# Kernel optimization log

Hardware: AMD Instinct MI355X
Metric: run time of the kernel (lower is better)

## Reference

```python
import jax, jax.numpy as jnp
import numpy as np
from jax import lax

EPSILON = 0.05      # sinkhorn entropic regularization (module init arg)
N_SINKHORN = 100    # fixed iteration count (POT default numItermax=1000 w/ early stop 1e-9)


def setup_inputs() -> dict:
    key = jax.random.key(0)
    k1, k2, k3 = jax.random.split(key, 3)
    B, D = 2048, 1024
    audio_emb = jax.random.normal(k1, (B, D), dtype=jnp.float32)
    text_emb = jax.random.normal(k2, (B, D), dtype=jnp.float32)
    # learned metric L (set via set_L); PSD so diag(L) > 0 and sqrt is real
    A = jax.random.normal(k3, (D, D), dtype=jnp.float32)
    L = (A @ A.T) / jnp.float32(D)
    return {"audio_emb": audio_emb, "text_emb": text_emb, "L": L}


def reference(audio_emb, text_emb, L):
    B = audio_emb.shape[0]
    M = jnp.nan_to_num(L)
    # SVD is computed in the original (reg term), but the final loss discards it
    s = jnp.linalg.svd(M, compute_uv=False)
    _reg = jnp.sum(s)  # unused in returned loss (original: loss = wloss)

    # einsum('ijk,ikj,kk->ij') only reads diag(M):
    # M_dist[i,j] = sum_k diag(M)[k] * (audio[j,k] - text[i,k])^2
    w = jnp.diagonal(M)  # [D]
    aw = jnp.einsum('jd,d->j', audio_emb * audio_emb, w)        # [B]
    tw = jnp.einsum('id,d->i', text_emb * text_emb, w)          # [B]
    cross = jnp.einsum('id,jd->ij', text_emb * w, audio_emb)    # [B,B]
    M_dist = tw[:, None] + aw[None, :] - 2.0 * cross
    M_dist = jnp.sqrt(jnp.maximum(M_dist, 0.0))
    M_dist = M_dist / jnp.max(M_dist)

    # Sinkhorn-Knopp (ot.sinkhorn, method='sinkhorn')
    a = jnp.ones((B,), dtype=M_dist.dtype) / B
    b = jnp.ones((B,), dtype=M_dist.dtype) / B
    K = jnp.exp(-M_dist / EPSILON)  # [B,B]

    def step(uv, _):
        u, v = uv
        v = b / (K.T @ u)
        u = a / (K @ v)
        return (u, v), None

    u0 = jnp.ones((B,), dtype=M_dist.dtype) / B
    v0 = jnp.ones((B,), dtype=M_dist.dtype) / B
    (u, v), _ = lax.scan(step, (u0, v0), None, length=N_SINKHORN)
    # pi = diag(u) K diag(v); pi_hat = eye(B)/B -> only diag(pi) matters
    pi_diag = u * jnp.diagonal(K) * v  # [B]
    wloss = -jnp.sum(jnp.log(pi_diag)) / B
    return wloss
```

## Files before the change

kernel.cpp:

```cpp
#include <hip/hip_runtime.h>
#include <hip/hip_fp16.h>
#include <math.h>

#define NB 2048
#define ND 1024
#define EPS 0.05f
#define NITER 100
#define SBLK 256
#define KSCALE 16384.0f
#define LOG_KSCALE 9.704060527839234

typedef float f32x4 __attribute__((ext_vector_type(4)));
typedef float f32x2 __attribute__((ext_vector_type(2)));
typedef short s16x8 __attribute__((ext_vector_type(8)));
typedef unsigned short u16x4 __attribute__((ext_vector_type(4)));
union Uh { f32x4 f; __half2 h[4]; };

__global__ void prep_k(const float* __restrict__ L, float* __restrict__ w,
                       float* __restrict__ u, float* __restrict__ v,
                       unsigned* __restrict__ maxbits, unsigned* __restrict__ flags) {
    int gtid = blockIdx.x * 256 + threadIdx.x;
    if (gtid < ND) {
        float x = L[(size_t)gtid * (ND + 1)];
        if (x != x) x = 0.f;
        else if (fabsf(x) == INFINITY) x = (x > 0.f) ? 3.4028235e38f : -3.4028235e38f;
        w[gtid] = x;
    }
    u[gtid] = 1.0f / NB;
    v[gtid] = 1.0f / NB;
    if (gtid == 0) *maxbits = 0u;
    if (gtid < 1024) flags[gtid] = 0u;
}

__global__ __launch_bounds__(256) void rows_k(const float* __restrict__ audio,
                                              const float* __restrict__ text,
                                              const float* __restrict__ w,
                                              float* __restrict__ aw, float* __restrict__ tw) {
    int r = blockIdx.x, tid = threadIdx.x;
    float4 wv = *(const float4*)&w[tid * 4];
    float4 a4 = *(const float4*)&audio[(size_t)r * ND + tid * 4];
    float4 t4 = *(const float4*)&text[(size_t)r * ND + tid * 4];
    float sa = a4.x * a4.x * wv.x + a4.y * a4.y * wv.y + a4.z * a4.z * wv.z + a4.w * a4.w * wv.w;
    float st = t4.x * t4.x * wv.x + t4.y * t4.y * wv.y + t4.z * t4.z * wv.z + t4.w * t4.w * wv.w;
    #pragma unroll
    for (int off = 32; off; off >>= 1) {
        sa += __shfl_down(sa, off, 64);
        st += __shfl_down(st, off, 64);
    }
    __shared__ float red[8];
    if ((tid & 63) == 0) { red[tid >> 6] = sa; red[4 + (tid >> 6)] = st; }
    __syncthreads();
    if (tid == 0) {
        aw[r] = red[0] + red[1] + red[2] + red[3];
        tw[r] = red[4] + red[5] + red[6] + red[7];
    }
}

__device__ __forceinline__ unsigned short f2bf(float x) {
    unsigned uu = __float_as_uint(x);
    return (unsigned short)((uu + 0x7FFFu + ((uu >> 16) & 1u)) >> 16);
}

__global__ __launch_bounds__(256) void gemm_mdist(
        const float* __restrict__ Tm, const float* __restrict__ Am,
        const float* __restrict__ wd, const float* __restrict__ tw, const float* __restrict__ aw,
        __half* __restrict__ Md, __half* __restrict__ MdT,
        float* __restrict__ diagMd, unsigned* __restrict__ maxbits) {
    __shared__ __align__(16) unsigned char smem[38912];
    float* wl = (float*)(smem + 34816);
    const int t = threadIdx.x;
    const int row0 = blockIdx.y * 128, col0 = blockIdx.x * 128;
    *(f32x4*)&wl[t * 4] = *(const f32x4*)&wd[t * 4];
    const int wv = t >> 6;
    const int wr = wv >> 1, wc = wv & 1;
    const int l = t & 63, lr = l & 15, kg = l >> 4;
    const int trow = t >> 4, tk4 = t & 15;
    const int px = (((tk4 >> 1) ^ (trow & 7)) << 4) + ((tk4 & 1) << 3);
    f32x4 acc[4][4];
    #pragma unroll
    for (int m = 0; m < 4; ++m)
        #pragma unroll
        for (int n = 0; n < 4; ++n) acc[m][n] = (f32x4){0.f, 0.f, 0.f, 0.f};
    __syncthreads();
    const float* tp = Tm + (size_t)(row0 + trow) * ND + tk4 * 4;
    const float* ap = Am + (size_t)(col0 + trow) * ND + tk4 * 4;
    for (int k0 = 0; k0 < ND; k0 += 64) {
        f32x4 wv4 = *(const f32x4*)&wl[k0 + tk4 * 4];
        __syncthreads();
        #pragma unroll
        for (int s = 0; s < 8; ++s) {
            f32x4 tv = *(const f32x4*)(tp + (size_t)(s * 16) * ND + k0);
            f32x4 av = *(const f32x4*)(ap + (size_t)(s * 16) * ND + k0);
            tv *= wv4;
            u16x4 tb, ab;
            tb[0] = f2bf(tv[0]); tb[1] = f2bf(tv[1]); tb[2] = f2bf(tv[2]); tb[3] = f2bf(tv[3]);
            ab[0] = f2bf(av[0]); ab[1] = f2bf(av[1]); ab[2] = f2bf(av[2]); ab[3] = f2bf(av[3]);
            const int rb = (s * 16 + trow) * 128 + px;
            *(u16x4*)(smem + rb) = tb;
            *(u16x4*)(smem + 16384 + rb) = ab;
        }
        __syncthreads();
        #pragma unroll
        for (int kk = 0; kk < 2; ++kk) {
            const int sl = (((kk << 2) + kg) ^ (lr & 7)) << 4;
            s16x8 af[4], bfr[4];
            #pragma unroll
            for (int m = 0; m < 4; ++m)
                af[m] = *(const s16x8*)(smem + (wr * 64 + m * 16 + lr) * 128 + sl);
            #pragma unroll
            for (int n = 0; n < 4; ++n)
                bfr[n] = *(const s16x8*)(smem + 16384 + (wc * 64 + n * 16 + lr) * 128 + sl);
            #pragma unroll
            for (int m = 0; m < 4; ++m)
                #pragma unroll
                for (int n = 0; n < 4; ++n)
                    acc[m][n] = __builtin_amdgcn_mfma_f32_16x16x32_bf16(af[m], bfr[n], acc[m][n], 0, 0, 0);
        }
    }
    __syncthreads();
    unsigned short* tr = (unsigned short*)smem;
    unsigned short* mdp = (unsigned short*)Md;
    float lmax = 0.f;
    #pragma unroll
    for (int m = 0; m < 4; ++m) {
        #pragma unroll
        for (int r = 0; r < 4; ++r) {
            const int li = wr * 64 + m * 16 + kg * 4 + r;
            const int i = row0 + li;
            const float twi = tw[i];
            #pragma unroll
            for (int n = 0; n < 4; ++n) {
                const int lj = wc * 64 + n * 16 + lr;
                const int j = col0 + lj;
                float md = twi + aw[j] - 2.0f * acc[m][n][r];
                md = sqrtf(fmaxf(md, 0.f));
                lmax = fmaxf(lmax, md);
                const unsigned short hb = __half_as_ushort(__float2half(md));
                mdp[(size_t)i * NB + j] = hb;
                tr[lj * 136 + li] = hb;
                if (i == j) diagMd[i] = md;
            }
        }
    }
    __syncthreads();
    {
        const int jj = t >> 1, ih = (t & 1) * 64;
        unsigned short* dst = (unsigned short*)MdT + (size_t)(col0 + jj) * NB + row0 + ih;
        #pragma unroll
        for (int x = 0; x < 8; ++x)
            *(s16x8*)(dst + x * 8) = *(const s16x8*)&tr[jj * 136 + ih + x * 8];
    }
    #pragma unroll
    for (int off = 32; off; off >>= 1) lmax = fmaxf(lmax, __shfl_down(lmax, off, 64));
    float* red = (float*)(smem + 34816);
    if (l == 0) red[t >> 6] = lmax;
    __syncthreads();
    if (t == 0) {
        float m2 = fmaxf(fmaxf(red[0], red[1]), fmaxf(red[2], red[3]));
        atomicMax(maxbits, __float_as_uint(m2));
    }
}

__global__ __launch_bounds__(256) void expconv_k(__half* __restrict__ Kall,
                                                 const unsigned* __restrict__ maxbits) {
    const float mx = __uint_as_float(*maxbits);
    const float cc = -1.0f / (mx * EPS);
    size_t idx = ((size_t)blockIdx.x * 256 + threadIdx.x) << 3;
    Uh uu; uu.f = *(const f32x4*)(Kall + idx);
    #pragma unroll
    for (int q = 0; q < 4; ++q) {
        float2 f = __half22float2(uu.h[q]);
        f.x = __expf(f.x * cc) * KSCALE;
        f.y = __expf(f.y * cc) * KSCALE;
        uu.h[q] = __floats2half2_rn(f.x, f.y);
    }
    *(f32x4*)(Kall + idx) = uu.f;
}

__device__ __forceinline__ void wait_phase(const unsigned* __restrict__ flags, int w, int l,
                                           unsigned ph) {
    if (w == 0) {
        const unsigned* p = flags + (l << 2);
        for (;;) {
            unsigned f0, f1, f2, f3;
            asm volatile("global_load_dword %0, %4, off sc0 sc1\n\t"
                         "global_load_dword %1, %5, off sc0 sc1\n\t"
                         "global_load_dword %2, %6, off sc0 sc1\n\t"
                         "global_load_dword %3, %7, off sc0 sc1\n\t"
                         "s_waitcnt vmcnt(0)"
                         : "=&v"(f0), "=&v"(f1), "=&v"(f2), "=&v"(f3)
                         : "v"(p), "v"(p + 256), "v"(p + 512), "v"(p + 768) : "memory");
            if (__all((f0 >= ph) && (f1 >= ph) && (f2 >= ph) && (f3 >= ph))) break;
            __builtin_amdgcn_s_sleep(1);
        }
    }
}

__device__ __forceinline__ void stage(const float* __restrict__ src, float* sv, int tid) {
    const float* p0 = src + (tid << 3);
    f32x4 r0, r1;
    asm volatile("global_load_dwordx4 %0, %2, off sc0 sc1\n\t"
                 "global_load_dwordx4 %1, %3, off sc0 sc1\n\t"
                 "s_waitcnt vmcnt(0)"
                 : "=&v"(r0), "=&v"(r1) : "v"(p0), "v"(p0 + 4) : "memory");
    *(f32x4*)&sv[tid * 12] = r0;
    *(f32x4*)&sv[tid * 12 + 4] = r1;
}

__device__ __forceinline__ void half_step_reg(const f32x4 (&kreg)[2][8],
                                              float* __restrict__ xout,
                                              const float* sv, int row0, float ab, int l) {
    float acc0 = 0.f, acc1 = 0.f;
    #pragma unroll
    for (int c = 0; c < 4; ++c) {
        const int col = (c << 9) + (l << 3);
        const int phys = col + ((col >> 3) << 2);
        f32x4 s0 = *(const f32x4*)&sv[phys];
        f32x4 s1 = *(const f32x4*)&sv[phys + 4];
        #pragma unroll
        for (int q = 0; q < 4; ++q) {
            acc0 = fmaf(kreg[0][2 * c][q], s0[q], acc0);
            acc0 = fmaf(kreg[0][2 * c + 1][q], s1[q], acc0);
            acc1 = fmaf(kreg[1][2 * c][q], s0[q], acc1);
            acc1 = fmaf(kreg[1][2 * c + 1][q], s1[q], acc1);
        }
    }
    #pragma unroll
    for (int off = 32; off; off >>= 1) {
        acc0 += __shfl_down(acc0, off, 64);
        acc1 += __shfl_down(acc1, off, 64);
    }
    if (l == 0) {
        f32x2 o;
        o[0] = ab / acc0; o[1] = ab / acc1;
        asm volatile("global_store_dwordx2 %1, %0, off sc0 sc1"
                     :: "v"(o), "v"(xout + row0) : "memory");
    }
    asm volatile("s_waitcnt vmcnt(0)" ::: "memory");
}

__global__ __launch_bounds__(256, 1) void sinkhorn_k(
        const __half* __restrict__ Kr, const __half* __restrict__ Kc,
        float* __restrict__ u, float* __restrict__ v,
        unsigned* __restrict__ flags) {
    __shared__ __align__(16) float sv[3072];
    const int tid = threadIdx.x, bid = blockIdx.x;
    const int w = tid >> 6, l = tid & 63;
    const int row0 = (bid << 3) + (w << 1);
    const float ab = 1.0f / NB;
    unsigned* myflag = flags + (bid << 2);
    f32x4 kc[2][8], kr[2][8];
    #pragma unroll
    for (int r = 0; r < 2; ++r) {
        const __half* pc = Kc + (size_t)(row0 + r) * NB;
        const __half* pr = Kr + (size_t)(row0 + r) * NB;
        #pragma unroll
        for (int c = 0; c < 4; ++c) {
            const int col = (c << 9) + (l << 3);
            Uh a; a.f = *(const f32x4*)(pc + col);
            Uh b; b.f = *(const f32x4*)(pr + col);
            float2 a0 = __half22float2(a.h[0]), a1 = __half22float2(a.h[1]);
            float2 a2 = __half22float2(a.h[2]), a3 = __half22float2(a.h[3]);
            float2 b0 = __half22float2(b.h[0]), b1 = __half22float2(b.h[1]);
            float2 b2 = __half22float2(b.h[2]), b3 = __half22float2(b.h[3]);
            kc[r][2 * c]     = (f32x4){a0.x, a0.y, a1.x, a1.y};
            kc[r][2 * c + 1] = (f32x4){a2.x, a2.y, a3.x, a3.y};
            kr[r][2 * c]     = (f32x4){b0.x, b0.y, b1.x, b1.y};
            kr[r][2 * c + 1] = (f32x4){b2.x, b2.y, b3.x, b3.y};
        }
    }
    for (int it = 0; it < NITER; ++it) {
        wait_phase(flags, w, l, 2 * it);
        __syncthreads();
        stage(u, sv, tid);
        __syncthreads();
        half_step_reg(kc, v, sv, row0, ab, l);
        __syncthreads();
        if (tid == 0) {
            unsigned ph = 2 * it + 1;
            asm volatile("global_store_dword %1, %0, off sc0 sc1"
                         :: "v"(ph), "v"(myflag) : "memory");
        }
        wait_phase(flags, w, l, 2 * it + 1);
        __syncthreads();
        stage(v, sv, tid);
        __syncthreads();
        half_step_reg(kr, u, sv, row0, ab, l);
        __syncthreads();
        if (tid == 0) {
            unsigned ph = 2 * it + 2;
            asm volatile("global_store_dword %1, %0, off sc0 sc1"
                         :: "v"(ph), "v"(myflag) : "memory");
        }
    }
}

__global__ void loss_k(const float* __restrict__ u, const float* __restrict__ v,
                       const float* __restrict__ diagMd, const unsigned* __restrict__ maxbits,
                       float* __restrict__ out) {
    int tid = threadIdx.x;
    float mx = __uint_as_float(*maxbits);
    float cc = 1.0f / (mx * EPS);
    double s = 0.0;
    for (int i = tid; i < NB; i += 256)
        s += (double)(logf(u[i]) + logf(v[i]) - diagMd[i] * cc);
    #pragma unroll
    for (int off = 32; off; off >>= 1) s += __shfl_down(s, off, 64);
    __shared__ double red[4];
    if ((tid & 63) == 0) red[tid >> 6] = s;
    __syncthreads();
    if (tid == 0)
        out[0] = (float)(-(red[0] + red[1] + red[2] + red[3]) / (double)NB - LOG_KSCALE);
}

extern "C" void kernel_launch(void* const* d_in, const int* in_sizes, int n_in,
                              void* d_out, int out_size, void* d_ws, size_t ws_size,
                              hipStream_t stream) {
    const float* audio = (const float*)d_in[0];
    const float* text  = (const float*)d_in[1];
    const float* L     = (const float*)d_in[2];
    char* ws = (char*)d_ws;
    float*    w       = (float*)(ws + 0);
    float*    aw      = (float*)(ws + 4096);
    float*    tw      = (float*)(ws + 12288);
    float*    u       = (float*)(ws + 20480);
    float*    v       = (float*)(ws + 28672);
    float*    diagMd  = (float*)(ws + 36864);
    unsigned* maxbits = (unsigned*)(ws + 45056);
    unsigned* flags   = (unsigned*)(ws + 45312);
    __half*   Md      = (__half*)(ws + 65536);
    __half*   MdT     = (__half*)(ws + 65536 + (size_t)NB * NB * 2);

    prep_k<<<8, 256, 0, stream>>>(L, w, u, v, maxbits, flags);
    rows_k<<<NB, 256, 0, stream>>>(audio, text, w, aw, tw);
    gemm_mdist<<<dim3(16, 16), 256, 0, stream>>>(text, audio, w, tw, aw, Md, MdT, diagMd, maxbits);
    expconv_k<<<4096, 256, 0, stream>>>(Md, maxbits);
    sinkhorn_k<<<SBLK, 256, 0, stream>>>(Md, MdT, u, v, flags);
    loss_k<<<1, 256, 0, stream>>>(u, v, diagMd, maxbits, (float*)d_out);
}
```

Measured before the change: 721.9 us.

## Fuse exp conversion into sinkhorn load and drop LDS staging of vectors

The separate expconv kernel is removed: sinkhorn_k now reads the fp16 normalized distances and applies exp in fp32 while loading them into registers, so the K-scale factor and its log correction disappear. In the iteration loop every wave now polls the flags itself and loads the full u/v vector straight from global memory into registers, replacing the shared-memory staging and two block barriers. This saves one kernel launch, a full read/write pass over the matrices, and per-iteration barriers. In exchange each wave issues redundant global loads and flag polls.

```diff
diff --git a/kernel.cpp b/kernel.cpp
--- a/kernel.cpp
+++ b/kernel.cpp
@@ -7,8 +7,6 @@
 #define EPS 0.05f
 #define NITER 100
 #define SBLK 256
-#define KSCALE 16384.0f
-#define LOG_KSCALE 9.704060527839234
 
 typedef float f32x4 __attribute__((ext_vector_type(4)));
 typedef float f32x2 __attribute__((ext_vector_type(2)));
@@ -161,68 +159,50 @@
     }
 }
 
-__global__ __launch_bounds__(256) void expconv_k(__half* __restrict__ Kall,
-                                                 const unsigned* __restrict__ maxbits) {
-    const float mx = __uint_as_float(*maxbits);
-    const float cc = -1.0f / (mx * EPS);
-    size_t idx = ((size_t)blockIdx.x * 256 + threadIdx.x) << 3;
-    Uh uu; uu.f = *(const f32x4*)(Kall + idx);
-    #pragma unroll
-    for (int q = 0; q < 4; ++q) {
-        float2 f = __half22float2(uu.h[q]);
-        f.x = __expf(f.x * cc) * KSCALE;
-        f.y = __expf(f.y * cc) * KSCALE;
-        uu.h[q] = __floats2half2_rn(f.x, f.y);
-    }
-    *(f32x4*)(Kall + idx) = uu.f;
-}
-
-__device__ __forceinline__ void wait_phase(const unsigned* __restrict__ flags, int w, int l,
+__device__ __forceinline__ void wait_phase(const unsigned* __restrict__ flags, int l,
                                            unsigned ph) {
-    if (w == 0) {
-        const unsigned* p = flags + (l << 2);
-        for (;;) {
-            unsigned f0, f1, f2, f3;
-            asm volatile("global_load_dword %0, %4, off sc0 sc1\n\t"
-                         "global_load_dword %1, %5, off sc0 sc1\n\t"
-                         "global_load_dword %2, %6, off sc0 sc1\n\t"
-                         "global_load_dword %3, %7, off sc0 sc1\n\t"
-                         "s_waitcnt vmcnt(0)"
-                         : "=&v"(f0), "=&v"(f1), "=&v"(f2), "=&v"(f3)
-                         : "v"(p), "v"(p + 256), "v"(p + 512), "v"(p + 768) : "memory");
-            if (__all((f0 >= ph) && (f1 >= ph) && (f2 >= ph) && (f3 >= ph))) break;
-            __builtin_amdgcn_s_sleep(1);
-        }
-    }
-}
-
-__device__ __forceinline__ void stage(const float* __restrict__ src, float* sv, int tid) {
-    const float* p0 = src + (tid << 3);
-    f32x4 r0, r1;
-    asm volatile("global_load_dwordx4 %0, %2, off sc0 sc1\n\t"
-                 "global_load_dwordx4 %1, %3, off sc0 sc1\n\t"
+    const unsigned* p = flags + (l << 2);
+    for (;;) {
+        unsigned f0, f1, f2, f3;
+        asm volatile("global_load_dword %0, %4, off sc0 sc1\n\t"
+                     "global_load_dword %1, %5, off sc0 sc1\n\t"
+                     "global_load_dword %2, %6, off sc0 sc1\n\t"
+                     "global_load_dword %3, %7, off sc0 sc1\n\t"
+                     "s_waitcnt vmcnt(0)"
+                     : "=&v"(f0), "=&v"(f1), "=&v"(f2), "=&v"(f3)
+                     : "v"(p), "v"(p + 256), "v"(p + 512), "v"(p + 768) : "memory");
+        if (__all((f0 >= ph) && (f1 >= ph) && (f2 >= ph) && (f3 >= ph))) break;
+        __builtin_amdgcn_s_sleep(1);
+    }
+}
+
+__device__ __forceinline__ void half_step_reg(const f32x4 (&kreg)[2][8],
+                                              const float* __restrict__ xin,
+                                              float* __restrict__ xout,
+                                              int row0, float ab, int l) {
+    const float* p0 = xin + (l << 3);
+    f32x4 x[8];
+    asm volatile("global_load_dwordx4 %0, %8, off sc0 sc1\n\t"
+                 "global_load_dwordx4 %1, %9, off sc0 sc1\n\t"
+                 "global_load_dwordx4 %2, %10, off sc0 sc1\n\t"
+                 "global_load_dwordx4 %3, %11, off sc0 sc1\n\t"
+                 "global_load_dwordx4 %4, %12, off sc0 sc1\n\t"
+                 "global_load_dwordx4 %5, %13, off sc0 sc1\n\t"
+                 "global_load_dwordx4 %6, %14, off sc0 sc1\n\t"
+                 "global_load_dwordx4 %7, %15, off sc0 sc1\n\t"
                  "s_waitcnt vmcnt(0)"
-                 : "=&v"(r0), "=&v"(r1) : "v"(p0), "v"(p0 + 4) : "memory");
-    *(f32x4*)&sv[tid * 12] = r0;
-    *(f32x4*)&sv[tid * 12 + 4] = r1;
-}
-
-__device__ __forceinline__ void half_step_reg(const f32x4 (&kreg)[2][8],
-                                              float* __restrict__ xout,
-                                              const float* sv, int row0, float ab, int l) {
+                 : "=&v"(x[0]), "=&v"(x[1]), "=&v"(x[2]), "=&v"(x[3]),
+                   "=&v"(x[4]), "=&v"(x[5]), "=&v"(x[6]), "=&v"(x[7])
+                 : "v"(p0), "v"(p0 + 4), "v"(p0 + 512), "v"(p0 + 516),
+                   "v"(p0 + 1024), "v"(p0 + 1028), "v"(p0 + 1536), "v"(p0 + 1540)
+                 : "memory");
     float acc0 = 0.f, acc1 = 0.f;
     #pragma unroll
-    for (int c = 0; c < 4; ++c) {
-        const int col = (c << 9) + (l << 3);
-        const int phys = col + ((col >> 3) << 2);
-        f32x4 s0 = *(const f32x4*)&sv[phys];
-        f32x4 s1 = *(const f32x4*)&sv[phys + 4];
+    for (int j = 0; j < 8; ++j) {
         #pragma unroll
         for (int q = 0; q < 4; ++q) {
-            acc0 = fmaf(kreg[0][2 * c][q], s0[q], acc0);
-            acc0 = fmaf(kreg[0][2 * c + 1][q], s1[q], acc0);
-            acc1 = fmaf(kreg[1][2 * c][q], s0[q], acc1);
-            acc1 = fmaf(kreg[1][2 * c + 1][q], s1[q], acc1);
+            acc0 = fmaf(kreg[0][j][q], x[j][q], acc0);
+            acc1 = fmaf(kreg[1][j][q], x[j][q], acc1);
         }
     }
     #pragma unroll
@@ -240,52 +220,48 @@
 }
 
 __global__ __launch_bounds__(256, 1) void sinkhorn_k(
-        const __half* __restrict__ Kr, const __half* __restrict__ Kc,
+        const __half* __restrict__ Mdr, const __half* __restrict__ Mdc,
         float* __restrict__ u, float* __restrict__ v,
-        unsigned* __restrict__ flags) {
-    __shared__ __align__(16) float sv[3072];
+        const unsigned* __restrict__ maxbits, unsigned* __restrict__ flags) {
     const int tid = threadIdx.x, bid = blockIdx.x;
     const int w = tid >> 6, l = tid & 63;
     const int row0 = (bid << 3) + (w << 1);
     const float ab = 1.0f / NB;
     unsigned* myflag = flags + (bid << 2);
+    const float mx = __uint_as_float(*maxbits);
+    const float cc = -1.0f / (mx * EPS);
     f32x4 kc[2][8], kr[2][8];
     #pragma unroll
     for (int r = 0; r < 2; ++r) {
-        const __half* pc = Kc + (size_t)(row0 + r) * NB;
-        const __half* pr = Kr + (size_t)(row0 + r) * NB;
+        const __half* pc = Mdc + (size_t)(row0 + r) * NB;
+        const __half* pr = Mdr + (size_t)(row0 + r) * NB;
         #pragma unroll
         for (int c = 0; c < 4; ++c) {
             const int col = (c << 9) + (l << 3);
             Uh a; a.f = *(const f32x4*)(pc + col);
             Uh b; b.f = *(const f32x4*)(pr + col);
-            float2 a0 = __half22float2(a.h[0]), a1 = __half22float2(a.h[1]);
-            float2 a2 = __half22float2(a.h[2]), a3 = __half22float2(a.h[3]);
-            float2 b0 = __half22float2(b.h[0]), b1 = __half22float2(b.h[1]);
-            float2 b2 = __half22float2(b.h[2]), b3 = __half22float2(b.h[3]);
-            kc[r][2 * c]     = (f32x4){a0.x, a0.y, a1.x, a1.y};
-            kc[r][2 * c + 1] = (f32x4){a2.x, a2.y, a3.x, a3.y};
-            kr[r][2 * c]     = (f32x4){b0.x, b0.y, b1.x, b1.y};
-            kr[r][2 * c + 1] = (f32x4){b2.x, b2.y, b3.x, b3.y};
+            #pragma unroll
+            for (int q = 0; q < 4; ++q) {
+                float2 fa = __half22float2(a.h[q]);
+                float2 fb = __half22float2(b.h[q]);
+                kc[r][2 * c + (q >> 1)][(q & 1) * 2]     = __expf(fa.x * cc);
+                kc[r][2 * c + (q >> 1)][(q & 1) * 2 + 1] = __expf(fa.y * cc);
+                kr[r][2 * c + (q >> 1)][(q & 1) * 2]     = __expf(fb.x * cc);
+                kr[r][2 * c + (q >> 1)][(q & 1) * 2 + 1] = __expf(fb.y * cc);
+            }
         }
     }
     for (int it = 0; it < NITER; ++it) {
-        wait_phase(flags, w, l, 2 * it);
-        __syncthreads();
-        stage(u, sv, tid);
-        __syncthreads();
-        half_step_reg(kc, v, sv, row0, ab, l);
+        wait_phase(flags, l, 2 * it);
+        half_step_reg(kc, u, v, row0, ab, l);
         __syncthreads();
         if (tid == 0) {
             unsigned ph = 2 * it + 1;
             asm volatile("global_store_dword %1, %0, off sc0 sc1"
                          :: "v"(ph), "v"(myflag) : "memory");
         }
-        wait_phase(flags, w, l, 2 * it + 1);
-        __syncthreads();
-        stage(v, sv, tid);
-        __syncthreads();
-        half_step_reg(kr, u, sv, row0, ab, l);
+        wait_phase(flags, l, 2 * it + 1);
+        half_step_reg(kr, v, u, row0, ab, l);
         __syncthreads();
         if (tid == 0) {
             unsigned ph = 2 * it + 2;
@@ -310,7 +286,7 @@
     if ((tid & 63) == 0) red[tid >> 6] = s;
     __syncthreads();
     if (tid == 0)
-        out[0] = (float)(-(red[0] + red[1] + red[2] + red[3]) / (double)NB - LOG_KSCALE);
+        out[0] = (float)(-(red[0] + red[1] + red[2] + red[3]) / (double)NB);
 }
 
 extern "C" void kernel_launch(void* const* d_in, const int* in_sizes, int n_in,
@@ -334,7 +310,6 @@
     prep_k<<<8, 256, 0, stream>>>(L, w, u, v, maxbits, flags);
     rows_k<<<NB, 256, 0, stream>>>(audio, text, w, aw, tw);
     gemm_mdist<<<dim3(16, 16), 256, 0, stream>>>(text, audio, w, tw, aw, Md, MdT, diagMd, maxbits);
-    expconv_k<<<4096, 256, 0, stream>>>(Md, maxbits);
-    sinkhorn_k<<<SBLK, 256, 0, stream>>>(Md, MdT, u, v, flags);
+    sinkhorn_k<<<SBLK, 256, 0, stream>>>(Md, MdT, u, v, maxbits, flags);
     loss_k<<<1, 256, 0, stream>>>(u, v, diagMd, maxbits, (float*)d_out);
 }
```

After: 713.8 us (median of 2 runs). No clear change (-1.1%).
